# Kernel tuning notes

Hardware: AMD Instinct MI355X
Metric: run time of the kernel (lower is better)

Reference implementation:

```python
import jax, jax.numpy as jnp
import numpy as np

NUM_SAMPLES = 50

def _sample_bezier(cp, t):
    # cp: [4, 2], t: [S, 1] -> [S, 2]
    p0, p1, p2, p3 = cp[0], cp[1], cp[2], cp[3]
    return ((1 - t) ** 3 * p0 + 3 * (1 - t) ** 2 * t * p1
            + 3 * (1 - t) * t ** 2 * p2 + t ** 3 * p3)

def setup_inputs() -> dict:
    key = jax.random.key(0)
    k1, k2, k3 = jax.random.split(key, 3)
    num_strokes = 64
    return {
        "strokes": jax.random.uniform(k1, (num_strokes, 4, 2), dtype=jnp.float32),
        "stroke_widths": jax.random.uniform(k2, (num_strokes,), dtype=jnp.float32) * 2.0 + 1.0,
        "stroke_colors": jax.random.uniform(k3, (num_strokes, 3), dtype=jnp.float32),
        "canvas_size": 512,
    }

def reference(strokes, stroke_widths, stroke_colors, canvas_size):
    H = W = canvas_size
    t = jnp.linspace(0.0, 1.0, NUM_SAMPLES, dtype=strokes.dtype)[:, None]  # [S,1]
    # sample all curves: [num_strokes, S, 2], scaled to pixel coords
    points = jax.vmap(lambda cp: _sample_bezier(cp, t))(strokes) * canvas_size
    coords = jnp.arange(canvas_size, dtype=strokes.dtype)
    yy, xx = jnp.meshgrid(coords, coords, indexing="ij")
    grid = jnp.stack([xx, yy], axis=-1)  # [H, W, 2]

    def composite(canvas, inp):
        pts, width, color = inp  # [S,2], [], [3]
        diff = grid[:, :, None, :] - pts[None, None, :, :]      # [H, W, S, 2]
        dist = jnp.sqrt(jnp.sum(diff * diff, axis=-1))           # [H, W, S]
        min_dist = jnp.min(dist, axis=-1)                        # [H, W]
        alpha = jax.nn.sigmoid((width - min_dist) * 2.0)         # [H, W]
        alpha = alpha[None, None]                                # [1,1,H,W]
        color_map = color[None, :, None, None]                   # [1,3,1,1]
        canvas = canvas * (1.0 - alpha) + color_map * alpha
        return canvas, None

    canvas0 = jnp.ones((1, 3, H, W), dtype=strokes.dtype)
    canvas, _ = jax.lax.scan(composite, canvas0, (points, stroke_widths, stroke_colors))
    return canvas
```

## Files before the change

kernel.cpp:

```cpp
#include <hip/hip_runtime.h>

#define NSTROKES 64
#define NSAMP    50
#define CANVAS   512
#define HW       (CANVAS * CANVAS)
#define TPB      1024
#define SPW      (NSTROKES / 16)
#define LSTRIDE  64

__global__ __launch_bounds__(TPB, 8) void raster_fused_kernel(
    const float* __restrict__ strokes,
    const float* __restrict__ widths,
    const float* __restrict__ colors,
    float* __restrict__ out)
{
    __shared__ __align__(16) float2 slist[NSTROKES * LSTRIDE];
    __shared__ unsigned int smask[NSTROKES];
    __shared__ float4       scol [NSTROKES];

    const int tid  = threadIdx.x;
    const int wave = tid >> 6;
    const int lane = tid & 63;
    const int px   = tid & 511;
    const int grp  = tid >> 9;
    const int y    = blockIdx.x;
    const float fy = (float)y;

    #pragma unroll
    for (int i = 0; i < SPW; ++i) {
        const int s = wave * SPW + i;

        float4 a = ((const float4*)strokes)[s * 2];
        float4 b = ((const float4*)strokes)[s * 2 + 1];
        const float S = (float)CANVAS;
        float c0x = a.x * S;
        float c1x = 3.0f * (a.z - a.x) * S;
        float c2x = 3.0f * (b.x - 2.0f * a.z + a.x) * S;
        float c3x = (b.z - 3.0f * b.x + 3.0f * a.z - a.x) * S;
        float c0y = a.y * S;
        float c1y = 3.0f * (a.w - a.y) * S;
        float c2y = 3.0f * (b.y - 2.0f * a.w + a.y) * S;
        float c3y = (b.w - 3.0f * b.y + 3.0f * a.w - a.y) * S;

        float w   = widths[s];
        float cut = w + 10.0f;

        float t   = (float)lane * (1.0f / (float)(NSAMP - 1));
        float px_ = fmaf(fmaf(fmaf(c3x, t, c2x), t, c1x), t, c0x);
        float py_ = fmaf(fmaf(fmaf(c3y, t, c2y), t, c1y), t, c0y);

        bool keep = (lane < NSAMP) && (fabsf(py_ - fy) <= cut);
        unsigned long long kmask = __ballot(keep);
        int idx = __popcll(kmask & ((1ull << lane) - 1ull));
        if (keep) {
            slist[s * LSTRIDE + idx] = make_float2(px_, py_);
        } else if (lane >= NSAMP) {
            slist[s * LSTRIDE + idx + (lane - NSAMP)] = make_float2(1e15f, 1e15f);
        }

        const int k0 = ((int)fmaxf(px_ - cut, 0.0f))   >> 6;
        const int k1 = ((int)fminf(px_ + cut, 511.0f)) >> 6;
        unsigned int mb = 0u;
        #pragma unroll
        for (int bb = 0; bb < 8; ++bb)
            mb |= (__ballot(keep && (k0 <= bb) && (bb <= k1)) != 0ull)
                      ? (1u << bb) : 0u;

        if (lane == 0) {
            smask[s] = ((unsigned int)__popcll(kmask) << 8) | mb;
            scol [s] = make_float4(colors[3*s], colors[3*s+1],
                                   colors[3*s+2], w);
        }
    }
    __syncthreads();

    const float fx    = (float)px;
    const int   sg    = wave & 7;
    const int   sbase = grp << 5;

    const unsigned int hdr_l = smask[sbase + (lane & 31)];
    unsigned int live = (unsigned int)__ballot((hdr_l >> sg) & 1u);

    float A = 1.0f, br = 0.0f, bg = 0.0f, bb = 0.0f;

    while (live) {
        const int s0 = sbase + (__ffs(live) - 1);
        live &= live - 1u;
        const bool has1 = (live != 0u);
        const int s1 = has1 ? (sbase + (__ffs(live) - 1)) : s0;
        if (has1) live &= live - 1u;

        const unsigned int h0 = smask[s0];
        const unsigned int h1 = smask[s1];
        float4 col0 = scol[s0];
        float4 col1 = scol[s1];
        const int   kc0 = (int)(h0 >> 8);
        const int   kc1 = has1 ? (int)(h1 >> 8) : 0;
        const float w0  = col0.w;
        const float w1  = col1.w;

        float m0 = 1e30f, m1 = 1e30f;
        const float4* L0 = (const float4*)(slist + s0 * LSTRIDE);
        const float4* L1 = (const float4*)(slist + s1 * LSTRIDE);

        const int kmax = kc0 > kc1 ? kc0 : kc1;
        for (int j = 0; j < kmax; j += 4) {
            if (j < kc0) {
                float4 q0 = L0[(j >> 1)];
                float4 q1 = L0[(j >> 1) + 1];
                float dy0 = fy - q0.y, dy1 = fy - q0.w;
                float dy2 = fy - q1.y, dy3 = fy - q1.w;
                float d0  = fx - q0.x, d1  = fx - q0.z;
                float d2  = fx - q1.x, d3  = fx - q1.z;
                float a01 = fminf(fmaf(d0, d0, dy0*dy0), fmaf(d1, d1, dy1*dy1));
                float a23 = fminf(fmaf(d2, d2, dy2*dy2), fmaf(d3, d3, dy3*dy3));
                m0 = fminf(fminf(a01, a23), m0);
            }
            if (j < kc1) {
                float4 q0 = L1[(j >> 1)];
                float4 q1 = L1[(j >> 1) + 1];
                float dy0 = fy - q0.y, dy1 = fy - q0.w;
                float dy2 = fy - q1.y, dy3 = fy - q1.w;
                float d0  = fx - q0.x, d1  = fx - q0.z;
                float d2  = fx - q1.x, d3  = fx - q1.z;
                float a01 = fminf(fmaf(d0, d0, dy0*dy0), fmaf(d1, d1, dy1*dy1));
                float a23 = fminf(fmaf(d2, d2, dy2*dy2), fmaf(d3, d3, dy3*dy3));
                m1 = fminf(fminf(a01, a23), m1);
            }
        }

        float al0 = __builtin_amdgcn_rcpf(1.0f + __expf(2.0f * (sqrtf(m0) - w0)));
        float al1 = __builtin_amdgcn_rcpf(1.0f + __expf(2.0f * (sqrtf(m1) - w1)));

        A  *= (1.0f - al0);
        br  = fmaf(al0, col0.x - br, br);
        bg  = fmaf(al0, col0.y - bg, bg);
        bb  = fmaf(al0, col0.z - bb, bb);
        if (has1) {
            A  *= (1.0f - al1);
            br  = fmaf(al1, col1.x - br, br);
            bg  = fmaf(al1, col1.y - bg, bg);
            bb  = fmaf(al1, col1.z - bb, bb);
        }
    }

    __syncthreads();
    float4* xfer = (float4*)slist;
    if (grp == 0) {
        xfer[px] = make_float4(A, br, bg, bb);
    }
    __syncthreads();
    if (grp == 1) {
        float4 g0 = xfer[px];
        float cr = fmaf(A, g0.x + g0.y, br);
        float cg = fmaf(A, g0.x + g0.z, bg);
        float cb = fmaf(A, g0.x + g0.w, bb);
        const int base = y * CANVAS + px;
        out[0*HW + base] = cr;
        out[1*HW + base] = cg;
        out[2*HW + base] = cb;
    }
}

extern "C" void kernel_launch(void* const* d_in, const int* in_sizes, int n_in,
                              void* d_out, int out_size, void* d_ws, size_t ws_size,
                              hipStream_t stream) {
    const float* strokes = (const float*)d_in[0];
    const float* widths  = (const float*)d_in[1];
    const float* colors  = (const float*)d_in[2];
    float* out = (float*)d_out;

    raster_fused_kernel<<<dim3(CANVAS), dim3(TPB), 0, stream>>>(
        strokes, widths, colors, out);
}
```

Baseline: 18.48 us.

## Use atomic work-queue of 16-stroke span units with half-precision partial compositing

Replaces the fixed split, in which each wave handles one 64-pixel span across 32 strokes, with a dynamic queue of 32 units, each covering 16 strokes and one span. Waves claim units through a shared atomic counter. This is meant to balance the uneven per-stroke work between waves. Each unit stores its partial (A, r, g, b) result as half2 in shared memory, and 512 threads then combine the four chunks in order. Using fp16 for the partial values adds rounding error to the output and costs an extra reduction step.

```diff
diff --git a/kernel.cpp b/kernel.cpp
--- a/kernel.cpp
+++ b/kernel.cpp
@@ -1,4 +1,5 @@
 #include <hip/hip_runtime.h>
+#include <hip/hip_fp16.h>
 
 #define NSTROKES 64
 #define NSAMP    50
@@ -7,6 +8,7 @@
 #define TPB      1024
 #define SPW      (NSTROKES / 16)
 #define LSTRIDE  64
+#define NUNITS   32
 
 __global__ __launch_bounds__(TPB, 8) void raster_fused_kernel(
     const float* __restrict__ strokes,
@@ -17,14 +19,16 @@
     __shared__ __align__(16) float2 slist[NSTROKES * LSTRIDE];
     __shared__ unsigned int smask[NSTROKES];
     __shared__ float4       scol [NSTROKES];
+    __shared__ __half2      hmap [NUNITS][64][2];
+    __shared__ int          uctr;
 
     const int tid  = threadIdx.x;
     const int wave = tid >> 6;
     const int lane = tid & 63;
-    const int px   = tid & 511;
-    const int grp  = tid >> 9;
     const int y    = blockIdx.x;
     const float fy = (float)y;
+
+    if (tid == 0) uctr = 0;
 
     #pragma unroll
     for (int i = 0; i < SPW; ++i) {
@@ -74,88 +78,103 @@
     }
     __syncthreads();
 
-    const float fx    = (float)px;
-    const int   sg    = wave & 7;
-    const int   sbase = grp << 5;
+    for (;;) {
+        int u = 0;
+        if (lane == 0) u = atomicAdd(&uctr, 1);
+        u = __shfl(u, 0);
+        if (u >= NUNITS) break;
 
-    const unsigned int hdr_l = smask[sbase + (lane & 31)];
-    unsigned int live = (unsigned int)__ballot((hdr_l >> sg) & 1u);
+        const int span  = u & 7;
+        const int sb    = (u >> 3) << 4;
+        const float fx  = (float)((span << 6) + lane);
 
-    float A = 1.0f, br = 0.0f, bg = 0.0f, bb = 0.0f;
+        const unsigned int hdr_l = smask[sb + (lane & 15)];
+        unsigned int live = (unsigned int)__ballot((hdr_l >> span) & 1u) & 0xFFFFu;
 
-    while (live) {
-        const int s0 = sbase + (__ffs(live) - 1);
-        live &= live - 1u;
-        const bool has1 = (live != 0u);
-        const int s1 = has1 ? (sbase + (__ffs(live) - 1)) : s0;
-        if (has1) live &= live - 1u;
+        float A = 1.0f, br = 0.0f, bg = 0.0f, bb = 0.0f;
 
-        const unsigned int h0 = smask[s0];
-        const unsigned int h1 = smask[s1];
-        float4 col0 = scol[s0];
-        float4 col1 = scol[s1];
-        const int   kc0 = (int)(h0 >> 8);
-        const int   kc1 = has1 ? (int)(h1 >> 8) : 0;
-        const float w0  = col0.w;
-        const float w1  = col1.w;
+        while (live) {
+            const int s0 = sb + (__ffs(live) - 1);
+            live &= live - 1u;
+            const bool has1 = (live != 0u);
+            const int s1 = has1 ? (sb + (__ffs(live) - 1)) : s0;
+            if (has1) live &= live - 1u;
 
-        float m0 = 1e30f, m1 = 1e30f;
-        const float4* L0 = (const float4*)(slist + s0 * LSTRIDE);
-        const float4* L1 = (const float4*)(slist + s1 * LSTRIDE);
+            const unsigned int h0 = smask[s0];
+            const unsigned int h1 = smask[s1];
+            float4 col0 = scol[s0];
+            float4 col1 = scol[s1];
+            const int   kc0 = (int)(h0 >> 8);
+            const int   kc1 = has1 ? (int)(h1 >> 8) : 0;
+            const float w0  = col0.w;
+            const float w1  = col1.w;
 
-        const int kmax = kc0 > kc1 ? kc0 : kc1;
-        for (int j = 0; j < kmax; j += 4) {
-            if (j < kc0) {
-                float4 q0 = L0[(j >> 1)];
-                float4 q1 = L0[(j >> 1) + 1];
-                float dy0 = fy - q0.y, dy1 = fy - q0.w;
-                float dy2 = fy - q1.y, dy3 = fy - q1.w;
-                float d0  = fx - q0.x, d1  = fx - q0.z;
-                float d2  = fx - q1.x, d3  = fx - q1.z;
-                float a01 = fminf(fmaf(d0, d0, dy0*dy0), fmaf(d1, d1, dy1*dy1));
-                float a23 = fminf(fmaf(d2, d2, dy2*dy2), fmaf(d3, d3, dy3*dy3));
-                m0 = fminf(fminf(a01, a23), m0);
+            float m0 = 1e30f, m1 = 1e30f;
+            const float4* L0 = (const float4*)(slist + s0 * LSTRIDE);
+            const float4* L1 = (const float4*)(slist + s1 * LSTRIDE);
+
+            const int kmax = kc0 > kc1 ? kc0 : kc1;
+            for (int j = 0; j < kmax; j += 4) {
+                if (j < kc0) {
+                    float4 q0 = L0[(j >> 1)];
+                    float4 q1 = L0[(j >> 1) + 1];
+                    float dy0 = fy - q0.y, dy1 = fy - q0.w;
+                    float dy2 = fy - q1.y, dy3 = fy - q1.w;
+                    float d0  = fx - q0.x, d1  = fx - q0.z;
+                    float d2  = fx - q1.x, d3  = fx - q1.z;
+                    float a01 = fminf(fmaf(d0,d0,dy0*dy0), fmaf(d1,d1,dy1*dy1));
+                    float a23 = fminf(fmaf(d2,d2,dy2*dy2), fmaf(d3,d3,dy3*dy3));
+                    m0 = fminf(fminf(a01, a23), m0);
+                }
+                if (j < kc1) {
+                    float4 q0 = L1[(j >> 1)];
+                    float4 q1 = L1[(j >> 1) + 1];
+                    float dy0 = fy - q0.y, dy1 = fy - q0.w;
+                    float dy2 = fy - q1.y, dy3 = fy - q1.w;
+                    float d0  = fx - q0.x, d1  = fx - q0.z;
+                    float d2  = fx - q1.x, d3  = fx - q1.z;
+                    float a01 = fminf(fmaf(d0,d0,dy0*dy0), fmaf(d1,d1,dy1*dy1));
+                    float a23 = fminf(fmaf(d2,d2,dy2*dy2), fmaf(d3,d3,dy3*dy3));
+                    m1 = fminf(fminf(a01, a23), m1);
+                }
             }
-            if (j < kc1) {
-                float4 q0 = L1[(j >> 1)];
-                float4 q1 = L1[(j >> 1) + 1];
-                float dy0 = fy - q0.y, dy1 = fy - q0.w;
-                float dy2 = fy - q1.y, dy3 = fy - q1.w;
-                float d0  = fx - q0.x, d1  = fx - q0.z;
-                float d2  = fx - q1.x, d3  = fx - q1.z;
-                float a01 = fminf(fmaf(d0, d0, dy0*dy0), fmaf(d1, d1, dy1*dy1));
-                float a23 = fminf(fmaf(d2, d2, dy2*dy2), fmaf(d3, d3, dy3*dy3));
-                m1 = fminf(fminf(a01, a23), m1);
+
+            float al0 = __builtin_amdgcn_rcpf(1.0f + __expf(2.0f*(sqrtf(m0)-w0)));
+            float al1 = __builtin_amdgcn_rcpf(1.0f + __expf(2.0f*(sqrtf(m1)-w1)));
+
+            A  *= (1.0f - al0);
+            br  = fmaf(al0, col0.x - br, br);
+            bg  = fmaf(al0, col0.y - bg, bg);
+            bb  = fmaf(al0, col0.z - bb, bb);
+            if (has1) {
+                A  *= (1.0f - al1);
+                br  = fmaf(al1, col1.x - br, br);
+                bg  = fmaf(al1, col1.y - bg, bg);
+                bb  = fmaf(al1, col1.z - bb, bb);
             }
         }
 
-        float al0 = __builtin_amdgcn_rcpf(1.0f + __expf(2.0f * (sqrtf(m0) - w0)));
-        float al1 = __builtin_amdgcn_rcpf(1.0f + __expf(2.0f * (sqrtf(m1) - w1)));
-
-        A  *= (1.0f - al0);
-        br  = fmaf(al0, col0.x - br, br);
-        bg  = fmaf(al0, col0.y - bg, bg);
-        bb  = fmaf(al0, col0.z - bb, bb);
-        if (has1) {
-            A  *= (1.0f - al1);
-            br  = fmaf(al1, col1.x - br, br);
-            bg  = fmaf(al1, col1.y - bg, bg);
-            bb  = fmaf(al1, col1.z - bb, bb);
-        }
-    }
-
-    __syncthreads();
-    float4* xfer = (float4*)slist;
-    if (grp == 0) {
-        xfer[px] = make_float4(A, br, bg, bb);
+        hmap[u][lane][0] = __floats2half2_rn(A,  br);
+        hmap[u][lane][1] = __floats2half2_rn(bg, bb);
     }
     __syncthreads();
-    if (grp == 1) {
-        float4 g0 = xfer[px];
-        float cr = fmaf(A, g0.x + g0.y, br);
-        float cg = fmaf(A, g0.x + g0.z, bg);
-        float cb = fmaf(A, g0.x + g0.w, bb);
-        const int base = y * CANVAS + px;
+
+    if (tid < 512) {
+        const int span = tid >> 6;
+        const int l    = tid & 63;
+
+        float cr = 1.0f, cg = 1.0f, cb = 1.0f;
+        #pragma unroll
+        for (int ck = 0; ck < 4; ++ck) {
+            const int u = (ck << 3) | span;
+            float2 p0 = __half22float2(hmap[u][l][0]);
+            float2 p1 = __half22float2(hmap[u][l][1]);
+            cr = fmaf(p0.x, cr, p0.y);
+            cg = fmaf(p0.x, cg, p1.x);
+            cb = fmaf(p0.x, cb, p1.y);
+        }
+
+        const int base = y * CANVAS + tid;
         out[0*HW + base] = cr;
         out[1*HW + base] = cg;
         out[2*HW + base] = cb;
```

New measurement: 18.80 us. Within noise of the previous version (+1.7%).
